# Optimization experiments

Hardware: AMD Instinct MI355X
Metric: run time of the kernel (lower is better)

## Reference

```python
import jax, jax.numpy as jnp
import numpy as np

IMAGE_SIZE = 224
PATCH_SIZE = 16
HALF_PATCH = PATCH_SIZE // 2
GRID = IMAGE_SIZE // PATCH_SIZE  # 14
NUM_PATCHES = GRID * GRID        # 196
C_IN = 3
C_CAT = 5 * C_IN                 # 15
PATCH_DIM = PATCH_SIZE * PATCH_SIZE * C_CAT  # 3840
PROJ_DIM = 768
EPS = 1e-6


def setup_inputs() -> dict:
    key = jax.random.key(0)
    k1, k2 = jax.random.split(key)
    images = jax.random.normal(k1, (64, IMAGE_SIZE, IMAGE_SIZE, C_IN), dtype=jnp.float32)
    W = jax.random.normal(k2, (PATCH_DIM, PROJ_DIM), dtype=jnp.float32) * 0.02
    b = jnp.zeros((PROJ_DIM,), dtype=jnp.float32)
    gamma = jnp.ones((PATCH_DIM,), dtype=jnp.float32)
    beta = jnp.zeros((PATCH_DIM,), dtype=jnp.float32)
    return {"images": images, "gamma": gamma, "beta": beta, "W": W, "b": b}


def _shift(images, crop_h, crop_w, shift_h, shift_w):
    S, hp = IMAGE_SIZE, HALF_PATCH
    # crop to (S-hp, S-hp) at (crop_h, crop_w), then pad back to (S, S) at (shift_h, shift_w)
    crop = images[:, crop_h:crop_h + S - hp, crop_w:crop_w + S - hp, :]
    return jnp.pad(crop, ((0, 0), (shift_h, hp - shift_h), (shift_w, hp - shift_w), (0, 0)))


def _forward(images, gamma, beta, W, b):
    hp = HALF_PATCH
    x = jnp.concatenate([
        images,
        _shift(images, hp, hp, 0, 0),   # left-up
        _shift(images, 0, hp, hp, 0),   # left-down
        _shift(images, hp, 0, 0, hp),   # right-up
        _shift(images, 0, 0, hp, hp),   # right-down
    ], axis=-1)  # [B, S, S, 15]
    B = x.shape[0]
    # non-overlapping patch extraction (tf.image.extract_patches, VALID, stride=patch)
    patches = (x.reshape(B, GRID, PATCH_SIZE, GRID, PATCH_SIZE, C_CAT)
                 .transpose(0, 1, 3, 2, 4, 5)
                 .reshape(B, GRID, GRID, PATCH_DIM))  # [B, 14, 14, 3840]
    flat = patches.reshape(B, NUM_PATCHES, PATCH_DIM)
    mean = jnp.mean(flat, axis=-1, keepdims=True)
    var = jnp.mean(jnp.square(flat - mean), axis=-1, keepdims=True)
    normed = (flat - mean) * jax.lax.rsqrt(var + EPS) * gamma + beta
    tokens = jnp.einsum('bnd,de->bne', normed, W) + b  # [B, 196, 768]
    return tokens, patches


def reference(images, gamma, beta, W, b):
    return _forward(images, gamma, beta, W, b)
```

## Files before the change

### kernel.cpp

```cpp
#include <hip/hip_runtime.h>
#include <hip/hip_bf16.h>

typedef unsigned short u16;
typedef unsigned int   u32;
typedef __attribute__((ext_vector_type(8))) short short8;
typedef __attribute__((ext_vector_type(4))) float floatx4;

#define IMG      224
#define GRIDD    14
#define NPATCH   12544
#define KDIM     3840
#define PROJ     768

__device__ __forceinline__ float b2f(u16 u) {
  union { u32 i; float f; } x; x.i = ((u32)u) << 16; return x.f;
}
__device__ __forceinline__ u16 f2b(float f) {
  union { u32 i; float f; } x; x.f = f;
  u32 r = x.i + 0x7fffu + ((x.i >> 16) & 1u);
  return (u16)(r >> 16);
}

__device__ __forceinline__ bool probe_bf16(const void* gamma) {
  return *(const u32*)gamma == 0x3F803F80u;
}
__device__ __forceinline__ float ldin(const void* p, size_t i, bool bf) {
  return bf ? b2f(((const u16*)p)[i]) : ((const float*)p)[i];
}

__device__ __forceinline__ void async_copy16(void* lds_uniform_base, const void* g) {
  __builtin_amdgcn_global_load_lds((const __attribute__((address_space(1))) u32*)g,
                                   (__attribute__((address_space(3))) u32*)lds_uniform_base,
                                   16, 0, 0);
}

struct alignas(8) us4 { u16 x, y, z, w; };

__global__ __launch_bounds__(256) void make_wg(const void* __restrict__ W,
                                               const void* __restrict__ gamma,
                                               const void* __restrict__ beta,
                                               u16* __restrict__ Wgt,
                                               float* __restrict__ u_arr,
                                               float* __restrict__ v_arr) {
  const bool bf = probe_bf16(gamma);
  __shared__ u16 tile[32][33];
  __shared__ float gs[32], bs[32];
  __shared__ float pu[8][33], pv[8][33];
  const int bx = blockIdx.x;
  const int by = blockIdx.y;
  const int tx = threadIdx.x;
  const int ty = threadIdx.y;
  if (ty == 0) {
    gs[tx] = ldin(gamma, by * 32 + tx, bf);
    bs[tx] = ldin(beta,  by * 32 + tx, bf);
  }
  __syncthreads();
  float ut = 0.f, vt = 0.f;
#pragma unroll
  for (int j = 0; j < 4; ++j) {
    const int a = ty + j * 8;
    const float wf = ldin(W, (size_t)(by * 32 + a) * PROJ + bx * 32 + tx, bf);
    ut += gs[a] * wf;
    vt += bs[a] * wf;
    tile[a][tx] = f2b(gs[a] * wf);
  }
  pu[ty][tx] = ut; pv[ty][tx] = vt;
  __syncthreads();
  if (ty == 0) {
    float su = 0.f, sv = 0.f;
#pragma unroll
    for (int t = 0; t < 8; ++t) { su += pu[t][tx]; sv += pv[t][tx]; }
    atomicAdd(&u_arr[bx * 32 + tx], su);
    atomicAdd(&v_arr[bx * 32 + tx], sv);
  }
#pragma unroll
  for (int j = 0; j < 4; ++j)
    Wgt[(size_t)(bx * 32 + ty + j * 8) * KDIM + by * 32 + tx] = tile[tx][ty + j * 8];
}

__global__ __launch_bounds__(256) void patch_stats(const void* __restrict__ images,
                                                   const void* __restrict__ gamma,
                                                   void* __restrict__ d_out,
                                                   float2* __restrict__ meaninv,
                                                   u16* __restrict__ Abf) {
  const bool bf = probe_bf16(gamma);
  const int p   = blockIdx.x;
  const int b   = p / 196;
  const int rem = p - b * 196;
  const int gy  = rem / GRIDD;
  const int gx  = rem - gy * GRIDD;
  const int tid = threadIdx.x;
  const int py  = tid >> 4, px = tid & 15;
  const int h   = gy * 16 + py, w = gx * 16 + px;

  __shared__ alignas(16) float vals[KDIM];
  __shared__ float red_s[4], red_q[4];

  const int dh[5] = {0, 8, -8, 8, -8};
  const int dw[5] = {0, 8, 8, -8, -8};

  float s = 0.f, q = 0.f;
#pragma unroll
  for (int g = 0; g < 5; ++g) {
    const int hh = h + dh[g], ww = w + dw[g];
    const bool ok = (hh >= 0) && (hh < IMG) && (ww >= 0) && (ww < IMG);
    const size_t base = ((size_t)(b * IMG + hh) * IMG + ww) * 3;
#pragma unroll
    for (int c = 0; c < 3; ++c) {
      const float f = ok ? ldin(images, base + c, bf) : 0.f;
      vals[tid * 15 + g * 3 + c] = f;
      s += f; q += f * f;
    }
  }

#pragma unroll
  for (int off = 32; off > 0; off >>= 1) {
    s += __shfl_down(s, off);
    q += __shfl_down(q, off);
  }
  const int wave = tid >> 6, lane = tid & 63;
  if (lane == 0) { red_s[wave] = s; red_q[wave] = q; }
  __syncthreads();
  const float S = red_s[0] + red_s[1] + red_s[2] + red_s[3];
  const float Q = red_q[0] + red_q[1] + red_q[2] + red_q[3];
  const float mean = S * (1.f / (float)KDIM);
  const float var  = Q * (1.f / (float)KDIM) - mean * mean;
  const float inv  = rsqrtf(var + 1e-6f);
  if (tid == 0) meaninv[p] = make_float2(mean, inv);

  const size_t pb = (size_t)p * KDIM;
  if (bf) {
    u16* po = (u16*)d_out + (size_t)NPATCH * PROJ;
    for (int i = tid; i < KDIM / 4; i += 256) {
      const int d = i * 4;
      us4 o;
      o.x = f2b(vals[d + 0]); o.y = f2b(vals[d + 1]);
      o.z = f2b(vals[d + 2]); o.w = f2b(vals[d + 3]);
      *(us4*)&po[pb + d] = o;
      if (Abf) *(us4*)&Abf[pb + d] = o;
    }
  } else {
    float* po = (float*)d_out + (size_t)NPATCH * PROJ;
    for (int i = tid; i < KDIM / 4; i += 256) {
      const int d = i * 4;
      *(float4*)&po[pb + d] = make_float4(vals[d + 0], vals[d + 1], vals[d + 2], vals[d + 3]);
      if (Abf) {
        us4 o;
        o.x = f2b(vals[d + 0]); o.y = f2b(vals[d + 1]);
        o.z = f2b(vals[d + 2]); o.w = f2b(vals[d + 3]);
        *(us4*)&Abf[pb + d] = o;
      }
    }
  }
}

__global__ __launch_bounds__(256) void gemm_ln_bf(const u16* __restrict__ Abf,
                                                  const u16* __restrict__ Wgt,
                                                  const float2* __restrict__ meaninv,
                                                  const float* __restrict__ u_arr,
                                                  const float* __restrict__ v_arr,
                                                  const void* __restrict__ bias,
                                                  const void* __restrict__ gamma,
                                                  void* __restrict__ d_out) {
  const bool bf = probe_bf16(gamma);
  __shared__ alignas(16) u16 As[128 * 32];
  __shared__ alignas(16) u16 Bs[128 * 32];
  __shared__ float2 mi[128];

  const int tid  = threadIdx.x;
  const int wave = tid >> 6, lane = tid & 63;
  const int cb = blockIdx.x;
  const int rb = blockIdx.y;

  const int m0 = (wave >> 1) * 64;
  const int n0 = (wave & 1) * 64;
  const int lr = lane & 15, quad = lane >> 4;

  if (tid < 128) mi[tid] = meaninv[rb * 128 + tid];

  floatx4 acc[4][4];
#pragma unroll
  for (int i = 0; i < 4; ++i)
#pragma unroll
    for (int j = 0; j < 4; ++j)
      acc[i][j] = (floatx4)0.f;

  const char* Ab = (const char*)Abf + (size_t)rb * 128 * (KDIM * 2);
  const char* Bb = (const char*)Wgt + (size_t)cb * 128 * (KDIM * 2);
  const int lrow = lane >> 2, lcol = (lane & 3) * 16;

  for (int kt = 0; kt < KDIM / 32; ++kt) {
    __syncthreads();
    const size_t kb = (size_t)kt * 64;
#pragma unroll
    for (int pass = 0; pass < 2; ++pass) {
      const int s = pass * 4 + wave;
      const int r = s * 16 + lrow;
      async_copy16((char*)As + s * 1024, Ab + (size_t)r * (KDIM * 2) + kb + lcol);
      async_copy16((char*)Bs + s * 1024, Bb + (size_t)r * (KDIM * 2) + kb + lcol);
    }
    __syncthreads();

    short8 af[4], bfr[4];
#pragma unroll
    for (int i = 0; i < 4; ++i)
      af[i] = *(const short8*)&As[(m0 + i * 16 + lr) * 32 + quad * 8];
#pragma unroll
    for (int j = 0; j < 4; ++j)
      bfr[j] = *(const short8*)&Bs[(n0 + j * 16 + lr) * 32 + quad * 8];
#pragma unroll
    for (int i = 0; i < 4; ++i)
#pragma unroll
      for (int j = 0; j < 4; ++j)
        acc[i][j] = __builtin_amdgcn_mfma_f32_16x16x32_bf16(af[i], bfr[j], acc[i][j], 0, 0, 0);
  }

#pragma unroll
  for (int j = 0; j < 4; ++j) {
    const int col = cb * 128 + n0 + j * 16 + lr;
    const float uc = u_arr[col];
    const float vc = v_arr[col] + ldin(bias, col, bf);
#pragma unroll
    for (int i = 0; i < 4; ++i) {
      const int rl0 = m0 + i * 16 + quad * 4;
#pragma unroll
      for (int t = 0; t < 4; ++t) {
        const float2 m = mi[rl0 + t];
        const float val = m.y * (acc[i][j][t] - m.x * uc) + vc;
        const size_t idx = (size_t)(rb * 128 + rl0 + t) * PROJ + col;
        if (bf) ((u16*)d_out)[idx] = f2b(val);
        else    ((float*)d_out)[idx] = val;
      }
    }
  }
}

__global__ __launch_bounds__(256) void gemm_ln_fp(const void* __restrict__ gamma,
                                                  const u16* __restrict__ Wgt,
                                                  const float2* __restrict__ meaninv,
                                                  const float* __restrict__ u_arr,
                                                  const float* __restrict__ v_arr,
                                                  const void* __restrict__ bias,
                                                  void* __restrict__ d_out) {
  const bool bf = probe_bf16(gamma);
  __shared__ alignas(16) u16 As[128 * 32];
  __shared__ alignas(16) u16 Bs[128 * 32];
  __shared__ float2 mi[128];

  const int tid  = threadIdx.x;
  const int wave = tid >> 6, lane = tid & 63;
  const int cb = blockIdx.x;
  const int rb = blockIdx.y;
  const int m0 = (wave >> 1) * 64;
  const int n0 = (wave & 1) * 64;
  const int lr = lane & 15, quad = lane >> 4;

  if (tid < 128) mi[tid] = meaninv[rb * 128 + tid];

  floatx4 acc[4][4];
#pragma unroll
  for (int i = 0; i < 4; ++i)
#pragma unroll
    for (int j = 0; j < 4; ++j)
      acc[i][j] = (floatx4)0.f;

  const char* patches2 = (const char*)d_out + (size_t)NPATCH * PROJ * 2;
  const char* patches4 = (const char*)d_out + (size_t)NPATCH * PROJ * 4;
  const char* Ab2 = patches2 + (size_t)rb * 128 * (KDIM * 2);
  const char* Ab4 = patches4 + (size_t)rb * 128 * (KDIM * 4);
  const char* Bb  = (const char*)Wgt + (size_t)cb * 128 * (KDIM * 2);

  for (int kt = 0; kt < KDIM / 32; ++kt) {
    __syncthreads();
    if (bf) {
#pragma unroll
      for (int pass = 0; pass < 2; ++pass) {
        const int o = pass * 4096 + tid * 16, r = o >> 6, cB = o & 63;
        *(uint4*)((char*)As + o) = *(const uint4*)(Ab2 + (size_t)r * (KDIM * 2) + kt * 64 + cB);
        *(uint4*)((char*)Bs + o) = *(const uint4*)(Bb  + (size_t)r * (KDIM * 2) + kt * 64 + cB);
      }
    } else {
#pragma unroll
      for (int pass = 0; pass < 2; ++pass) {
        const int o = pass * 4096 + tid * 16, r = o >> 6, cB = o & 63;
        const char* ga = Ab4 + (size_t)r * (KDIM * 4) + kt * 128 + cB * 2;
        const float4 f0 = *(const float4*)ga;
        const float4 f1 = *(const float4*)(ga + 16);
        union { uint4 qv; u16 hv[8]; } pk;
        pk.hv[0] = f2b(f0.x); pk.hv[1] = f2b(f0.y); pk.hv[2] = f2b(f0.z); pk.hv[3] = f2b(f0.w);
        pk.hv[4] = f2b(f1.x); pk.hv[5] = f2b(f1.y); pk.hv[6] = f2b(f1.z); pk.hv[7] = f2b(f1.w);
        *(uint4*)((char*)As + o) = pk.qv;
        *(uint4*)((char*)Bs + o) = *(const uint4*)(Bb + (size_t)r * (KDIM * 2) + kt * 64 + cB);
      }
    }
    __syncthreads();

    short8 af[4], bfr[4];
#pragma unroll
    for (int i = 0; i < 4; ++i)
      af[i] = *(const short8*)&As[(m0 + i * 16 + lr) * 32 + quad * 8];
#pragma unroll
    for (int j = 0; j < 4; ++j)
      bfr[j] = *(const short8*)&Bs[(n0 + j * 16 + lr) * 32 + quad * 8];
#pragma unroll
    for (int i = 0; i < 4; ++i)
#pragma unroll
      for (int j = 0; j < 4; ++j)
        acc[i][j] = __builtin_amdgcn_mfma_f32_16x16x32_bf16(af[i], bfr[j], acc[i][j], 0, 0, 0);
  }

#pragma unroll
  for (int j = 0; j < 4; ++j) {
    const int col = cb * 128 + n0 + j * 16 + lr;
    const float uc = u_arr[col];
    const float vc = v_arr[col] + ldin(bias, col, bf);
#pragma unroll
    for (int i = 0; i < 4; ++i) {
      const int rl0 = m0 + i * 16 + quad * 4;
#pragma unroll
      for (int t = 0; t < 4; ++t) {
        const float2 m = mi[rl0 + t];
        const float val = m.y * (acc[i][j][t] - m.x * uc) + vc;
        const size_t idx = (size_t)(rb * 128 + rl0 + t) * PROJ + col;
        if (bf) ((u16*)d_out)[idx] = f2b(val);
        else    ((float*)d_out)[idx] = val;
      }
    }
  }
}

extern "C" void kernel_launch(void* const* d_in, const int* in_sizes, int n_in,
                              void* d_out, int out_size, void* d_ws, size_t ws_size,
                              hipStream_t stream) {
  (void)in_sizes; (void)n_in; (void)out_size;
  const void* images = d_in[0];
  const void* gamma  = d_in[1];
  const void* beta   = d_in[2];
  const void* W      = d_in[3];
  const void* bias   = d_in[4];

  u16*    Wgt     = (u16*)d_ws;
  size_t  off     = (size_t)PROJ * KDIM * 2;
  float2* meaninv = (float2*)((char*)d_ws + off);
  off            += (size_t)NPATCH * 8;
  float*  u_arr   = (float*)((char*)d_ws + off);
  off            += PROJ * 4;
  float*  v_arr   = (float*)((char*)d_ws + off);
  off            += PROJ * 4;
  u16*    Abf     = (u16*)((char*)d_ws + off);
  const size_t need = off + (size_t)NPATCH * KDIM * 2;
  const bool useA = ws_size >= need;

  hipMemsetAsync(u_arr, 0, 2 * PROJ * sizeof(float), stream);
  hipLaunchKernelGGL(make_wg, dim3(24, 120), dim3(32, 8), 0, stream,
                     W, gamma, beta, Wgt, u_arr, v_arr);
  hipLaunchKernelGGL(patch_stats, dim3(NPATCH), dim3(256), 0, stream,
                     images, gamma, d_out, meaninv, useA ? Abf : (u16*)nullptr);
  if (useA)
    hipLaunchKernelGGL(gemm_ln_bf, dim3(6, 98), dim3(256), 0, stream,
                       Abf, Wgt, meaninv, u_arr, v_arr, bias, gamma, d_out);
  else
    hipLaunchKernelGGL(gemm_ln_fp, dim3(6, 98), dim3(256), 0, stream,
                       gamma, Wgt, meaninv, u_arr, v_arr, bias, d_out);
}
```

Baseline: 497.7 us.

## Double-buffer GEMM LDS tiles and remap blocks across XCDs

Splits the LDS A/B tiles into two buffers and issues the async global-to-LDS copy for the next K slice before the MFMA work on the current slice, leaving one barrier per iteration instead of two. It also remaps the linear block index so that consecutive tiles sharing A rows land on the same XCD, which should improve L2 reuse. The cost is twice the LDS per block, which may lower occupancy. The remap hard-codes a 98x6 grid split over 8 XCDs.

```diff
diff --git a/kernel.cpp b/kernel.cpp
--- a/kernel.cpp
+++ b/kernel.cpp
@@ -163,14 +163,19 @@
                                                   const void* __restrict__ gamma,
                                                   void* __restrict__ d_out) {
   const bool bf = probe_bf16(gamma);
-  __shared__ alignas(16) u16 As[128 * 32];
-  __shared__ alignas(16) u16 Bs[128 * 32];
+  __shared__ alignas(16) u16 As[2][128 * 32];
+  __shared__ alignas(16) u16 Bs[2][128 * 32];
   __shared__ float2 mi[128];
 
   const int tid  = threadIdx.x;
   const int wave = tid >> 6, lane = tid & 63;
-  const int cb = blockIdx.x;
-  const int rb = blockIdx.y;
+
+  const int lin  = blockIdx.y * 6 + blockIdx.x;
+  const int xcd  = lin & 7;
+  const int slot = lin >> 3;
+  const int v    = (xcd < 4 ? xcd * 74 : 296 + (xcd - 4) * 73) + slot;
+  const int rb   = v / 6;
+  const int cb   = v - rb * 6;
 
   const int m0 = (wave >> 1) * 64;
   const int n0 = (wave & 1) * 64;
@@ -189,31 +194,41 @@
   const char* Bb = (const char*)Wgt + (size_t)cb * 128 * (KDIM * 2);
   const int lrow = lane >> 2, lcol = (lane & 3) * 16;
 
+#define STAGE(kt, buf)                                                          \
+  {                                                                             \
+    const size_t kb_ = (size_t)(kt) * 64;                                       \
+    char* Ad_ = (char*)&As[(buf)][0];                                           \
+    char* Bd_ = (char*)&Bs[(buf)][0];                                           \
+    _Pragma("unroll")                                                           \
+    for (int pass = 0; pass < 2; ++pass) {                                      \
+      const int s_ = pass * 4 + wave;          \
+      const int r_ = s_ * 16 + lrow;                                            \
+      async_copy16(Ad_ + s_ * 1024, Ab + (size_t)r_ * (KDIM * 2) + kb_ + lcol); \
+      async_copy16(Bd_ + s_ * 1024, Bb + (size_t)r_ * (KDIM * 2) + kb_ + lcol); \
+    }                                                                           \
+  }
+
+  STAGE(0, 0);
+  __syncthreads();
+
   for (int kt = 0; kt < KDIM / 32; ++kt) {
-    __syncthreads();
-    const size_t kb = (size_t)kt * 64;
-#pragma unroll
-    for (int pass = 0; pass < 2; ++pass) {
-      const int s = pass * 4 + wave;
-      const int r = s * 16 + lrow;
-      async_copy16((char*)As + s * 1024, Ab + (size_t)r * (KDIM * 2) + kb + lcol);
-      async_copy16((char*)Bs + s * 1024, Bb + (size_t)r * (KDIM * 2) + kb + lcol);
-    }
-    __syncthreads();
-
+    const int cur = kt & 1;
+    if (kt + 1 < KDIM / 32) STAGE(kt + 1, cur ^ 1);
     short8 af[4], bfr[4];
 #pragma unroll
     for (int i = 0; i < 4; ++i)
-      af[i] = *(const short8*)&As[(m0 + i * 16 + lr) * 32 + quad * 8];
+      af[i] = *(const short8*)&As[cur][(m0 + i * 16 + lr) * 32 + quad * 8];
 #pragma unroll
     for (int j = 0; j < 4; ++j)
-      bfr[j] = *(const short8*)&Bs[(n0 + j * 16 + lr) * 32 + quad * 8];
+      bfr[j] = *(const short8*)&Bs[cur][(n0 + j * 16 + lr) * 32 + quad * 8];
 #pragma unroll
     for (int i = 0; i < 4; ++i)
 #pragma unroll
       for (int j = 0; j < 4; ++j)
         acc[i][j] = __builtin_amdgcn_mfma_f32_16x16x32_bf16(af[i], bfr[j], acc[i][j], 0, 0, 0);
-  }
+    __syncthreads();
+  }
+#undef STAGE
 
 #pragma unroll
   for (int j = 0; j < 4; ++j) {
```

Result: slower. 535.1 us (+7.5%).

## Stage padded image window in LDS and remap GEMM blocks by XCD

Applied to the files above, without the earlier changes.

The patch_stats kernel now loads a contiguous 32x96 padded window of the source image into shared memory with coalesced loads. It then gathers the five shifted copies from LDS, replacing scattered per-thread global loads of 3 floats at each of 5 offsets. The GEMM kernel also remaps its linear block index so that consecutive tiles land on the same XCD, which improves L2 reuse of A/W rows across the chiplets. Both changes add index arithmetic and an extra barrier, and the remap hardcodes a grid of 588 blocks split 74/73 per XCD.

```diff
diff --git a/kernel.cpp b/kernel.cpp
--- a/kernel.cpp
+++ b/kernel.cpp
@@ -90,28 +90,44 @@
   const int gy  = rem / GRIDD;
   const int gx  = rem - gy * GRIDD;
   const int tid = threadIdx.x;
-  const int py  = tid >> 4, px = tid & 15;
-  const int h   = gy * 16 + py, w = gx * 16 + px;
-
-  __shared__ alignas(16) float vals[KDIM];
+
+  __shared__ alignas(16) float buf[KDIM];
   __shared__ float red_s[4], red_q[4];
 
-  const int dh[5] = {0, 8, -8, 8, -8};
-  const int dw[5] = {0, 8, 8, -8, -8};
-
+  {
+    const int h0  = gy * 16 - 8;
+    const int wc0 = gx * 48 - 24;
+#pragma unroll
+    for (int k = 0; k < 12; ++k) {
+      const int f    = tid + k * 256;
+      const int t1   = f >> 5;
+      const int rrow = (t1 * 43691) >> 17;
+      const int colf = f - rrow * 96;
+      const int h    = h0 + rrow;
+      const int wc   = wc0 + colf;
+      const bool ok  = (h >= 0) && (h < IMG) && (wc >= 0) && (wc < IMG * 3);
+      buf[f] = ok ? ldin(images, (size_t)(b * IMG + h) * (IMG * 3) + wc, bf) : 0.f;
+    }
+  }
+  __syncthreads();
+
+  const int py = tid >> 4, px = tid & 15;
+  const int rbase = (py + 8) * 96 + (px + 8) * 3;
+  const int goff[5] = {0, 792, -744, 744, -792};
+  float r[15];
   float s = 0.f, q = 0.f;
 #pragma unroll
-  for (int g = 0; g < 5; ++g) {
-    const int hh = h + dh[g], ww = w + dw[g];
-    const bool ok = (hh >= 0) && (hh < IMG) && (ww >= 0) && (ww < IMG);
-    const size_t base = ((size_t)(b * IMG + hh) * IMG + ww) * 3;
+  for (int g = 0; g < 5; ++g)
 #pragma unroll
     for (int c = 0; c < 3; ++c) {
-      const float f = ok ? ldin(images, base + c, bf) : 0.f;
-      vals[tid * 15 + g * 3 + c] = f;
+      const float f = buf[rbase + goff[g] + c];
+      r[g * 3 + c] = f;
       s += f; q += f * f;
     }
-  }
+  __syncthreads();
+
+#pragma unroll
+  for (int j = 0; j < 15; ++j) buf[tid * 15 + j] = r[j];
 
 #pragma unroll
   for (int off = 32; off > 0; off >>= 1) {
@@ -121,6 +137,7 @@
   const int wave = tid >> 6, lane = tid & 63;
   if (lane == 0) { red_s[wave] = s; red_q[wave] = q; }
   __syncthreads();
+
   const float S = red_s[0] + red_s[1] + red_s[2] + red_s[3];
   const float Q = red_q[0] + red_q[1] + red_q[2] + red_q[3];
   const float mean = S * (1.f / (float)KDIM);
@@ -134,8 +151,8 @@
     for (int i = tid; i < KDIM / 4; i += 256) {
       const int d = i * 4;
       us4 o;
-      o.x = f2b(vals[d + 0]); o.y = f2b(vals[d + 1]);
-      o.z = f2b(vals[d + 2]); o.w = f2b(vals[d + 3]);
+      o.x = f2b(buf[d + 0]); o.y = f2b(buf[d + 1]);
+      o.z = f2b(buf[d + 2]); o.w = f2b(buf[d + 3]);
       *(us4*)&po[pb + d] = o;
       if (Abf) *(us4*)&Abf[pb + d] = o;
     }
@@ -143,11 +160,11 @@
     float* po = (float*)d_out + (size_t)NPATCH * PROJ;
     for (int i = tid; i < KDIM / 4; i += 256) {
       const int d = i * 4;
-      *(float4*)&po[pb + d] = make_float4(vals[d + 0], vals[d + 1], vals[d + 2], vals[d + 3]);
+      const float4 v = *(const float4*)&buf[d];
+      *(float4*)&po[pb + d] = v;
       if (Abf) {
         us4 o;
-        o.x = f2b(vals[d + 0]); o.y = f2b(vals[d + 1]);
-        o.z = f2b(vals[d + 2]); o.w = f2b(vals[d + 3]);
+        o.x = f2b(v.x); o.y = f2b(v.y); o.z = f2b(v.z); o.w = f2b(v.w);
         *(us4*)&Abf[pb + d] = o;
       }
     }
@@ -169,8 +186,13 @@
 
   const int tid  = threadIdx.x;
   const int wave = tid >> 6, lane = tid & 63;
-  const int cb = blockIdx.x;
-  const int rb = blockIdx.y;
+
+  const int lin  = blockIdx.y * 6 + blockIdx.x;
+  const int xcd  = lin & 7;
+  const int slot = lin >> 3;
+  const int v    = (xcd < 4 ? xcd * 74 : 296 + (xcd - 4) * 73) + slot;
+  const int rb   = v / 6;
+  const int cb   = v - rb * 6;
 
   const int m0 = (wave >> 1) * 64;
   const int n0 = (wave & 1) * 64;
```

New measurement: 517.2 us. +3.9%, slower.
